# Performance work log

Hardware: AMD Instinct MI355X
Metric: run time of the kernel (lower is better)

The kernel has to match this reference:

```python
import jax, jax.numpy as jnp
import numpy as np
import math

N_MENTIONS = 8192
EMB = 1024


def setup_inputs() -> dict:
    key = jax.random.key(0)
    k0, k1, k2 = jax.random.split(key, 3)
    scale = 1.0 / math.sqrt(EMB)
    return {
        "all_mentions": jax.random.normal(k0, (N_MENTIONS, EMB), dtype=jnp.float32),
        "Wq": jax.random.normal(k1, (EMB, EMB), dtype=jnp.float32) * scale,
        "bq": jnp.zeros((EMB,), dtype=jnp.float32),
        "Wk": jax.random.normal(k2, (EMB, EMB), dtype=jnp.float32) * scale,
        "bk": jnp.zeros((EMB,), dtype=jnp.float32),
    }


def reference(all_mentions, Wq, bq, Wk, bk):
    # torch.nn.Linear: y = x @ W.T + b
    E = all_mentions.shape[-1]
    q = (all_mentions @ Wq.T + bq) / jnp.sqrt(jnp.asarray(E, all_mentions.dtype))
    k = all_mentions @ Wk.T + bk
    # [N, N] raw attention logits
    attn = q @ k.T
    # causal mask: -inf strictly above the diagonal (triu, diagonal=1)
    n = all_mentions.shape[0]
    mask = jnp.where(jnp.triu(jnp.ones((n, n), dtype=bool), k=1),
                     jnp.asarray(-jnp.inf, attn.dtype),
                     jnp.asarray(0.0, attn.dtype))
    # Module returns attn_weights = masked pre-softmax logits (single layer,
    # single head, bsz=1); the softmax@v branch is discarded by the caller.
    return attn + mask
```

## Files before the change

kernel.cpp:

```cpp
#include <hip/hip_runtime.h>
#include <math.h>

#define NM 8192
#define KDIM 1024

#define NEG_BIG (-3.0e38f)

typedef __attribute__((ext_vector_type(4))) float floatx4;
typedef __attribute__((ext_vector_type(8))) _Float16 halfx8;
typedef __attribute__((ext_vector_type(4))) _Float16 halfx4;

#define SMEM_BYTES (3 * (256 * 64 + 128 * 64) * 2)

__device__ __forceinline__ void gload_lds16(const void* g, void* l) {
    __builtin_amdgcn_global_load_lds(
        (const __attribute__((address_space(1))) void*)g,
        (__attribute__((address_space(3))) void*)l,
        16, 0, 0);
}

__global__ __launch_bounds__(256)
void convert_kernel(const float* __restrict__ X,
                    const float* __restrict__ Wq,
                    const float* __restrict__ Wk,
                    _Float16* __restrict__ Xf,
                    _Float16* __restrict__ Wqf,
                    _Float16* __restrict__ Wkf) {
    const int XB = (NM * KDIM) / 4 / 256;
    const int WB = (KDIM * KDIM) / 4 / 256;
    int b = blockIdx.x;
    const float* src;
    _Float16* dst;
    if (b < XB)            { src = X;  dst = Xf; }
    else if (b < XB + WB)  { b -= XB;       src = Wq; dst = Wqf; }
    else                   { b -= XB + WB;  src = Wk; dst = Wkf; }
    const int i = b * 256 + threadIdx.x;
    floatx4 v = ((const floatx4*)src)[i];
    halfx4 h;
    h.x = (_Float16)v.x;
    h.y = (_Float16)v.y;
    h.z = (_Float16)v.z;
    h.w = (_Float16)v.w;
    *(halfx4*)&dst[(size_t)i * 4] = h;
}


#define GEMM_PIPE_BODY(APTR, BPTR)                                            \
    extern __shared__ _Float16 smem[];                                        \
    _Float16* const sAl = smem;                           \
    _Float16* const sBl = smem + 3 * 16384;               \
    const int t = threadIdx.x;                                                \
    const int lane = t & 63;                                                  \
    const int quad = lane >> 4;                                               \
    const int l15 = lane & 15;                                                \
    const int wv = t >> 6;                                                    \
    const int wr = (wv >> 1) * 64;                \
    const int wc = (wv & 1) * 64;                 \
    const int srow = t >> 3;             \
    const int skoff = ((t & 7) ^ ((t >> 3) & 7)) * 8;     \
    auto stA = [&](int kt, int pb, int c) {                                   \
        gload_lds16(APTR + (size_t)(row0 + c * 64 + srow) * KDIM              \
                         + kt * 64 + skoff,                                   \
                    sAl + pb * 16384 + (c * 512 + t) * 8);                    \
    };                                                                        \
    auto stB = [&](int kt, int pb, int c) {                                   \
        gload_lds16(BPTR + (size_t)(col0 + c * 64 + srow) * KDIM              \
                         + kt * 64 + skoff,                                   \
                    sBl + pb * 8192 + (c * 512 + t) * 8);                     \
    };                                                                        \
    floatx4 acc[4][4];                                                        \
    _Pragma("unroll")                                                         \
    for (int i = 0; i < 4; i++)                                               \
        _Pragma("unroll")                                                     \
        for (int j = 0; j < 4; j++) acc[i][j] = (floatx4){0.f, 0.f, 0.f, 0.f}; \
    stA(0, 0, 0); stA(0, 0, 1); stA(0, 0, 2); stA(0, 0, 3);                   \
    stB(0, 0, 0); stB(0, 0, 1);                                               \
    stA(1, 1, 0); stA(1, 1, 1); stA(1, 1, 2); stA(1, 1, 3);                   \
    stB(1, 1, 0); stB(1, 1, 1);                                               \
    asm volatile("s_waitcnt vmcnt(6)" ::: "memory");       \
    __builtin_amdgcn_s_barrier();                                             \
    _Pragma("unroll")                                                         \
    for (int kt = 0; kt < 16; ++kt) {                                         \
        const int pb = kt % 3;                                                \
        const int pq = (kt + 2) % 3;                                          \
        halfx8 a[4], b[4];                                                    \
                                              \
        if (kt < 14) { stA(kt + 2, pq, 0); stA(kt + 2, pq, 1);                \
                       stB(kt + 2, pq, 0); }                                  \
        _Pragma("unroll")                                                     \
        for (int i = 0; i < 4; i++) {                                         \
            const int r = wr + i * 16 + l15;                                  \
            a[i] = *(const halfx8*)&sAl[pb * 16384 + r * 64 +                 \
                                        ((quad ^ (r & 7)) * 8)];              \
        }                                                                     \
        _Pragma("unroll")                                                     \
        for (int j = 0; j < 4; j++) {                                         \
            const int r = wc + j * 16 + l15;                                  \
            b[j] = *(const halfx8*)&sBl[pb * 8192 + r * 64 +                  \
                                        ((quad ^ (r & 7)) * 8)];              \
        }                                                                     \
        __builtin_amdgcn_s_barrier();                                         \
        asm volatile("s_waitcnt lgkmcnt(0)" ::: "memory");                    \
        __builtin_amdgcn_sched_barrier(0);                                    \
        __builtin_amdgcn_s_setprio(1);                                        \
        _Pragma("unroll")                                                     \
        for (int j = 0; j < 4; j++)                                           \
            _Pragma("unroll")                                                 \
            for (int i = 0; i < 4; i++)                                       \
                acc[i][j] = __builtin_amdgcn_mfma_f32_16x16x32_f16(           \
                    a[i], b[j], acc[i][j], 0, 0, 0);                          \
        __builtin_amdgcn_s_setprio(0);                                        \
        __builtin_amdgcn_s_barrier();                                         \
                                              \
        if (kt < 14) { stA(kt + 2, pq, 2); stA(kt + 2, pq, 3);                \
                       stB(kt + 2, pq, 1); }                                  \
        _Pragma("unroll")                                                     \
        for (int i = 0; i < 4; i++) {                                         \
            const int r = wr + i * 16 + l15;                                  \
            a[i] = *(const halfx8*)&sAl[pb * 16384 + r * 64 +                 \
                                        (((4 + quad) ^ (r & 7)) * 8)];        \
        }                                                                     \
        _Pragma("unroll")                                                     \
        for (int j = 0; j < 4; j++) {                                         \
            const int r = wc + j * 16 + l15;                                  \
            b[j] = *(const halfx8*)&sBl[pb * 8192 + r * 64 +                  \
                                        (((4 + quad) ^ (r & 7)) * 8)];        \
        }                                                                     \
        __builtin_amdgcn_s_barrier();                                         \
        asm volatile("s_waitcnt lgkmcnt(0)" ::: "memory");                    \
        __builtin_amdgcn_sched_barrier(0);                                    \
        __builtin_amdgcn_s_setprio(1);                                        \
        _Pragma("unroll")                                                     \
        for (int j = 0; j < 4; j++)                                           \
            _Pragma("unroll")                                                 \
            for (int i = 0; i < 4; i++)                                       \
                acc[i][j] = __builtin_amdgcn_mfma_f32_16x16x32_f16(           \
                    a[i], b[j], acc[i][j], 0, 0, 0);                          \
        __builtin_amdgcn_s_setprio(0);                                        \
        if (kt < 14)       asm volatile("s_waitcnt vmcnt(6)" ::: "memory");   \
        else if (kt == 14) asm volatile("s_waitcnt vmcnt(0)" ::: "memory");   \
        if (kt < 15) __builtin_amdgcn_s_barrier();                            \
    }

__global__ __launch_bounds__(512, 2)
void proj_kernel(const _Float16* __restrict__ Xf,
                 const _Float16* __restrict__ Wqf, const float* __restrict__ bq,
                 _Float16* __restrict__ Qf,
                 const _Float16* __restrict__ Wkf, const float* __restrict__ bk,
                 _Float16* __restrict__ Kf) {
    const bool isK = (blockIdx.z == 1);
    const _Float16* W    = isK ? Wkf : Wqf;
    const float*    bias = isK ? bk : bq;
    _Float16*       O    = isK ? Kf : Qf;
    const float scale = isK ? 1.0f : 0.03125f;

    const int row0 = blockIdx.y * 256;
    const int col0 = blockIdx.x * 128;

    GEMM_PIPE_BODY(Xf, W)

#pragma unroll
    for (int i = 0; i < 4; i++)
#pragma unroll
        for (int j = 0; j < 4; j++)
#pragma unroll
            for (int r = 0; r < 4; r++) {
                const int grow = row0 + wr + i * 16 + quad * 4 + r;
                const int gcol = col0 + wc + j * 16 + l15;
                const float v = (acc[i][j][r] + bias[gcol]) * scale;
                O[(size_t)grow * KDIM + gcol] = (_Float16)v;
            }
}

__global__ __launch_bounds__(512, 2)
void attn_kernel(const _Float16* __restrict__ Qf,
                 const _Float16* __restrict__ Kf,
                 float* __restrict__ out) {
    const int lid = blockIdx.x;
    const int x = lid & 7;
    const int s = lid >> 3;
    const int bi = s & 31;
    const int bj = ((s >> 5) << 3) + x;

    if (bj * 128 > bi * 256 + 255) {
        const int tid = threadIdx.x;
        const floatx4 v = {NEG_BIG, NEG_BIG, NEG_BIG, NEG_BIG};
        floatx4* o4 = (floatx4*)(out + (size_t)bi * 256 * NM + (size_t)bj * 128);
#pragma unroll
        for (int it = 0; it < 16; ++it) {
            const int idx = it * 512 + tid;
            const int r = idx >> 5;
            const int c = idx & 31;
            __builtin_nontemporal_store(v, &o4[(size_t)r * (NM / 4) + c]);
        }
        return;
    }

    const int row0 = bi * 256;
    const int col0 = bj * 128;

    GEMM_PIPE_BODY(Qf, Kf)

#pragma unroll
    for (int i = 0; i < 4; i++)
#pragma unroll
        for (int j = 0; j < 4; j++)
#pragma unroll
            for (int r = 0; r < 4; r++) {
                const int grow = row0 + wr + i * 16 + quad * 4 + r;
                const int gcol = col0 + wc + j * 16 + l15;
                const float v = (gcol <= grow) ? acc[i][j][r] : NEG_BIG;
                __builtin_nontemporal_store(v, &out[(size_t)grow * NM + gcol]);
            }
}

extern "C" void kernel_launch(void* const* d_in, const int* in_sizes, int n_in,
                              void* d_out, int out_size, void* d_ws, size_t ws_size,
                              hipStream_t stream) {
    const float* X  = (const float*)d_in[0];
    const float* Wq = (const float*)d_in[1];
    const float* bq = (const float*)d_in[2];
    const float* Wk = (const float*)d_in[3];
    const float* bk = (const float*)d_in[4];
    float* out = (float*)d_out;

    _Float16* p = (_Float16*)d_ws;
    const size_t XN = (size_t)NM * KDIM;
    const size_t WN = (size_t)KDIM * KDIM;
    _Float16* Xf  = p;  p += XN;
    _Float16* Wqf = p;  p += WN;
    _Float16* Wkf = p;  p += WN;
    _Float16* Qf  = p;  p += XN;
    _Float16* Kf  = p;  p += XN;

    static bool attr_done = false;
    if (!attr_done) {
        hipFuncSetAttribute((const void*)proj_kernel,
                            hipFuncAttributeMaxDynamicSharedMemorySize, SMEM_BYTES);
        hipFuncSetAttribute((const void*)attn_kernel,
                            hipFuncAttributeMaxDynamicSharedMemorySize, SMEM_BYTES);
        attr_done = true;
    }

    const int nconv = (int)((XN + 2 * WN) / 4 / 256);
    convert_kernel<<<nconv, 256, 0, stream>>>(X, Wq, Wk, Xf, Wqf, Wkf);

    dim3 pgrid(KDIM / 128, NM / 256, 2);
    proj_kernel<<<pgrid, 512, SMEM_BYTES, stream>>>(Xf, Wqf, bq, Qf, Wkf, bk, Kf);

    attn_kernel<<<(NM / 256) * (NM / 128), 512, SMEM_BYTES, stream>>>(Qf, Kf, out);
}
```

Baseline: 434.4 us.

## Switch GEMMs to 256x256 tiles with 8-phase double-buffered pipeline

Both the projection and attention GEMMs move from 256x128 block tiles with a 3-stage LDS ring to 256x256 tiles with a 2-stage double buffer. Each K-tile is split into four phases that interleave LDS reads, async global-to-LDS staging and MFMA bursts. This raises arithmetic intensity per block and halves the number of blocks. The causal skip test becomes a block-level bj > bi check, and masking is applied only on diagonal tiles. In exchange it uses more accumulator registers, does coarser diagonal work, and the pipeline timing is tighter with only two buffers.

```diff
diff --git a/kernel.cpp b/kernel.cpp
--- a/kernel.cpp
+++ b/kernel.cpp
@@ -10,7 +10,7 @@
 typedef __attribute__((ext_vector_type(8))) _Float16 halfx8;
 typedef __attribute__((ext_vector_type(4))) _Float16 halfx4;
 
-#define SMEM_BYTES (3 * (256 * 64 + 128 * 64) * 2)
+#define SMEM_BYTES (2 * 2 * 256 * 64 * 2)
 
 __device__ __forceinline__ void gload_lds16(const void* g, void* l) {
     __builtin_amdgcn_global_load_lds(
@@ -45,101 +45,138 @@
 }
 
 
-#define GEMM_PIPE_BODY(APTR, BPTR)                                            \
+#define RD_A(d, i, kk)                                                        \
+    (*(const halfx8*)&smem[(d) * 32768 + ((i) >> 2) * 8192 +                  \
+                           (((i) & 3) * 32 + wm * 16 + l15) * 64 +            \
+                           ((((kk) * 4 + quad) ^ (l15 & 7)) * 8)])
+#define RD_B(d, j, kk)                                                        \
+    (*(const halfx8*)&smem[(d) * 32768 + 16384 + ((j) >> 1) * 8192 +          \
+                           (((j) & 1) * 64 + wn * 16 + l15) * 64 +            \
+                           ((((kk) * 4 + quad) ^ (l15 & 7)) * 8)])
+
+#define MFMA16(JLO, JHI, IOFF)                                                \
+    _Pragma("unroll")                                                         \
+    for (int jj = (JLO); jj < (JHI); ++jj)                                    \
+        _Pragma("unroll")                                                     \
+        for (int ii = 0; ii < 4; ++ii) {                                      \
+            acc[(IOFF) + ii][jj] = __builtin_amdgcn_mfma_f32_16x16x32_f16(    \
+                aR[ii][0], bR[jj][0], acc[(IOFF) + ii][jj], 0, 0, 0);         \
+            acc[(IOFF) + ii][jj] = __builtin_amdgcn_mfma_f32_16x16x32_f16(    \
+                aR[ii][1], bR[jj][1], acc[(IOFF) + ii][jj], 0, 0, 0);         \
+        }
+
+#define KTILE(d, STG1, STG2, STG3, STG4, VMTAIL)                              \
+    {                                                                         \
+                                                       \
+        _Pragma("unroll")                                                     \
+        for (int ii = 0; ii < 4; ++ii) {                                      \
+            aR[ii][0] = RD_A(d, ii, 0);                                       \
+            aR[ii][1] = RD_A(d, ii, 1);                                       \
+        }                                                                     \
+        _Pragma("unroll")                                                     \
+        for (int jj = 0; jj < 2; ++jj) {                                      \
+            bR[jj][0] = RD_B(d, jj, 0);                                       \
+            bR[jj][1] = RD_B(d, jj, 1);                                       \
+        }                                                                     \
+        STG1;                                                                 \
+        asm volatile("s_waitcnt lgkmcnt(8)" ::: "memory");                    \
+        __builtin_amdgcn_s_barrier();                                         \
+        asm volatile("s_waitcnt lgkmcnt(0)" ::: "memory");                    \
+        __builtin_amdgcn_sched_barrier(0);                                    \
+        __builtin_amdgcn_s_setprio(1);                                        \
+        MFMA16(0, 2, 0)                                                       \
+        __builtin_amdgcn_s_setprio(0);                                        \
+        __builtin_amdgcn_s_barrier();                                         \
+                                                       \
+        _Pragma("unroll")                                                     \
+        for (int jj = 2; jj < 4; ++jj) {                                      \
+            bR[jj][0] = RD_B(d, jj, 0);                                       \
+            bR[jj][1] = RD_B(d, jj, 1);                                       \
+        }                                                                     \
+        STG2;                                                                 \
+        __builtin_amdgcn_s_barrier();                                         \
+        asm volatile("s_waitcnt lgkmcnt(0)" ::: "memory");                    \
+        __builtin_amdgcn_sched_barrier(0);                                    \
+        __builtin_amdgcn_s_setprio(1);                                        \
+        MFMA16(2, 4, 0)                                                       \
+        __builtin_amdgcn_s_setprio(0);                                        \
+        __builtin_amdgcn_s_barrier();                                         \
+                                                       \
+        _Pragma("unroll")                                                     \
+        for (int ii = 0; ii < 4; ++ii) {                                      \
+            aR[ii][0] = RD_A(d, 4 + ii, 0);                                   \
+            aR[ii][1] = RD_A(d, 4 + ii, 1);                                   \
+        }                                                                     \
+        STG3;                                                                 \
+        __builtin_amdgcn_s_barrier();                                         \
+        asm volatile("s_waitcnt lgkmcnt(0)" ::: "memory");                    \
+        __builtin_amdgcn_sched_barrier(0);                                    \
+        __builtin_amdgcn_s_setprio(1);                                        \
+        MFMA16(0, 2, 4)                                                       \
+        __builtin_amdgcn_s_setprio(0);                                        \
+        __builtin_amdgcn_s_barrier();                                         \
+                                \
+        STG4;                                                                 \
+        __builtin_amdgcn_s_barrier();                                         \
+        __builtin_amdgcn_s_setprio(1);                                        \
+        MFMA16(2, 4, 4)                                                       \
+        __builtin_amdgcn_s_setprio(0);                                        \
+        VMTAIL;                                                               \
+        __builtin_amdgcn_s_barrier();                                         \
+    }
+
+#define GEMM_CORE_8PHASE(APTR, BPTR)                                          \
     extern __shared__ _Float16 smem[];                                        \
-    _Float16* const sAl = smem;                           \
-    _Float16* const sBl = smem + 3 * 16384;               \
     const int t = threadIdx.x;                                                \
     const int lane = t & 63;                                                  \
     const int quad = lane >> 4;                                               \
     const int l15 = lane & 15;                                                \
-    const int wv = t >> 6;                                                    \
-    const int wr = (wv >> 1) * 64;                \
-    const int wc = (wv & 1) * 64;                 \
-    const int srow = t >> 3;             \
-    const int skoff = ((t & 7) ^ ((t >> 3) & 7)) * 8;     \
-    auto stA = [&](int kt, int pb, int c) {                                   \
-        gload_lds16(APTR + (size_t)(row0 + c * 64 + srow) * KDIM              \
-                         + kt * 64 + skoff,                                   \
-                    sAl + pb * 16384 + (c * 512 + t) * 8);                    \
+    const int wm = (t >> 6) >> 2;                                             \
+    const int wn = (t >> 6) & 3;                                              \
+    const int srow8 = t >> 3;                                                 \
+    const int schunk = ((t & 7) ^ (srow8 & 7)) * 8;                           \
+    const _Float16* const aSrc = (APTR) + (size_t)(row0 + srow8) * KDIM + schunk; \
+    const _Float16* const bSrc = (BPTR) + (size_t)(col0 + srow8) * KDIM + schunk; \
+    auto STG_A = [&](int kt, int d, int h) {                                  \
+        _Pragma("unroll")                                                     \
+        for (int c = 0; c < 2; ++c)                                           \
+            gload_lds16(aSrc + (size_t)(h * 128 + c * 64) * KDIM + kt * 64,   \
+                        smem + d * 32768 + h * 8192 + (c * 512 + t) * 8);     \
     };                                                                        \
-    auto stB = [&](int kt, int pb, int c) {                                   \
-        gload_lds16(BPTR + (size_t)(col0 + c * 64 + srow) * KDIM              \
-                         + kt * 64 + skoff,                                   \
-                    sBl + pb * 8192 + (c * 512 + t) * 8);                     \
+    auto STG_B = [&](int kt, int d, int h) {                                  \
+        _Pragma("unroll")                                                     \
+        for (int c = 0; c < 2; ++c)                                           \
+            gload_lds16(bSrc + (size_t)(h * 128 + c * 64) * KDIM + kt * 64,   \
+                        smem + d * 32768 + 16384 + h * 8192 + (c * 512 + t) * 8); \
     };                                                                        \
-    floatx4 acc[4][4];                                                        \
+    floatx4 acc[8][4];                                                        \
     _Pragma("unroll")                                                         \
-    for (int i = 0; i < 4; i++)                                               \
+    for (int i = 0; i < 8; i++)                                               \
         _Pragma("unroll")                                                     \
         for (int j = 0; j < 4; j++) acc[i][j] = (floatx4){0.f, 0.f, 0.f, 0.f}; \
-    stA(0, 0, 0); stA(0, 0, 1); stA(0, 0, 2); stA(0, 0, 3);                   \
-    stB(0, 0, 0); stB(0, 0, 1);                                               \
-    stA(1, 1, 0); stA(1, 1, 1); stA(1, 1, 2); stA(1, 1, 3);                   \
-    stB(1, 1, 0); stB(1, 1, 1);                                               \
-    asm volatile("s_waitcnt vmcnt(6)" ::: "memory");       \
+    halfx8 aR[4][2], bR[4][2];                                                \
+          \
+    STG_A(0, 0, 0); STG_B(0, 0, 0); STG_B(0, 0, 1); STG_A(0, 0, 1);           \
+    STG_A(1, 1, 0); STG_B(1, 1, 0); STG_B(1, 1, 1);                           \
+    asm volatile("s_waitcnt vmcnt(6)" ::: "memory");          \
     __builtin_amdgcn_s_barrier();                                             \
-    _Pragma("unroll")                                                         \
-    for (int kt = 0; kt < 16; ++kt) {                                         \
-        const int pb = kt % 3;                                                \
-        const int pq = (kt + 2) % 3;                                          \
-        halfx8 a[4], b[4];                                                    \
-                                              \
-        if (kt < 14) { stA(kt + 2, pq, 0); stA(kt + 2, pq, 1);                \
-                       stB(kt + 2, pq, 0); }                                  \
-        _Pragma("unroll")                                                     \
-        for (int i = 0; i < 4; i++) {                                         \
-            const int r = wr + i * 16 + l15;                                  \
-            a[i] = *(const halfx8*)&sAl[pb * 16384 + r * 64 +                 \
-                                        ((quad ^ (r & 7)) * 8)];              \
-        }                                                                     \
-        _Pragma("unroll")                                                     \
-        for (int j = 0; j < 4; j++) {                                         \
-            const int r = wc + j * 16 + l15;                                  \
-            b[j] = *(const halfx8*)&sBl[pb * 8192 + r * 64 +                  \
-                                        ((quad ^ (r & 7)) * 8)];              \
-        }                                                                     \
-        __builtin_amdgcn_s_barrier();                                         \
-        asm volatile("s_waitcnt lgkmcnt(0)" ::: "memory");                    \
-        __builtin_amdgcn_sched_barrier(0);                                    \
-        __builtin_amdgcn_s_setprio(1);                                        \
-        _Pragma("unroll")                                                     \
-        for (int j = 0; j < 4; j++)                                           \
-            _Pragma("unroll")                                                 \
-            for (int i = 0; i < 4; i++)                                       \
-                acc[i][j] = __builtin_amdgcn_mfma_f32_16x16x32_f16(           \
-                    a[i], b[j], acc[i][j], 0, 0, 0);                          \
-        __builtin_amdgcn_s_setprio(0);                                        \
-        __builtin_amdgcn_s_barrier();                                         \
-                                              \
-        if (kt < 14) { stA(kt + 2, pq, 2); stA(kt + 2, pq, 3);                \
-                       stB(kt + 2, pq, 1); }                                  \
-        _Pragma("unroll")                                                     \
-        for (int i = 0; i < 4; i++) {                                         \
-            const int r = wr + i * 16 + l15;                                  \
-            a[i] = *(const halfx8*)&sAl[pb * 16384 + r * 64 +                 \
-                                        (((4 + quad) ^ (r & 7)) * 8)];        \
-        }                                                                     \
-        _Pragma("unroll")                                                     \
-        for (int j = 0; j < 4; j++) {                                         \
-            const int r = wc + j * 16 + l15;                                  \
-            b[j] = *(const halfx8*)&sBl[pb * 8192 + r * 64 +                  \
-                                        (((4 + quad) ^ (r & 7)) * 8)];        \
-        }                                                                     \
-        __builtin_amdgcn_s_barrier();                                         \
-        asm volatile("s_waitcnt lgkmcnt(0)" ::: "memory");                    \
-        __builtin_amdgcn_sched_barrier(0);                                    \
-        __builtin_amdgcn_s_setprio(1);                                        \
-        _Pragma("unroll")                                                     \
-        for (int j = 0; j < 4; j++)                                           \
-            _Pragma("unroll")                                                 \
-            for (int i = 0; i < 4; i++)                                       \
-                acc[i][j] = __builtin_amdgcn_mfma_f32_16x16x32_f16(           \
-                    a[i], b[j], acc[i][j], 0, 0, 0);                          \
-        __builtin_amdgcn_s_setprio(0);                                        \
-        if (kt < 14)       asm volatile("s_waitcnt vmcnt(6)" ::: "memory");   \
-        else if (kt == 14) asm volatile("s_waitcnt vmcnt(0)" ::: "memory");   \
-        if (kt < 15) __builtin_amdgcn_s_barrier();                            \
+    _Pragma("unroll 1")                                                       \
+    for (int it = 0; it < 8; ++it) {                                          \
+        const int kt1 = 2 * it + 1, kt2 = 2 * it + 2, kt3 = 2 * it + 3;       \
+        const bool stg = (it < 7);                                            \
+        KTILE(0,                                                              \
+              STG_A(kt1, 1, 1),                                               \
+              if (stg) STG_A(kt2, 0, 0),                                      \
+              if (stg) STG_B(kt2, 0, 0),                                      \
+              if (stg) STG_B(kt2, 0, 1),                                      \
+              if (stg) { asm volatile("s_waitcnt vmcnt(6)" ::: "memory"); }   \
+              else { asm volatile("s_waitcnt vmcnt(0)" ::: "memory"); })      \
+        KTILE(1,                                                              \
+              if (stg) STG_A(kt2, 0, 1),                                      \
+              if (stg) STG_A(kt3, 1, 0),                                      \
+              if (stg) STG_B(kt3, 1, 0),                                      \
+              if (stg) STG_B(kt3, 1, 1),                                      \
+              if (stg) { asm volatile("s_waitcnt vmcnt(6)" ::: "memory"); })  \
     }
 
 __global__ __launch_bounds__(512, 2)
@@ -155,19 +192,19 @@
     const float scale = isK ? 1.0f : 0.03125f;
 
     const int row0 = blockIdx.y * 256;
-    const int col0 = blockIdx.x * 128;
-
-    GEMM_PIPE_BODY(Xf, W)
-
-#pragma unroll
-    for (int i = 0; i < 4; i++)
+    const int col0 = blockIdx.x * 256;
+
+    GEMM_CORE_8PHASE(Xf, W)
+
+#pragma unroll
+    for (int i = 0; i < 8; i++)
 #pragma unroll
         for (int j = 0; j < 4; j++)
 #pragma unroll
-            for (int r = 0; r < 4; r++) {
-                const int grow = row0 + wr + i * 16 + quad * 4 + r;
-                const int gcol = col0 + wc + j * 16 + l15;
-                const float v = (acc[i][j][r] + bias[gcol]) * scale;
+            for (int rr = 0; rr < 4; rr++) {
+                const int grow = row0 + i * 32 + wm * 16 + quad * 4 + rr;
+                const int gcol = col0 + j * 64 + wn * 16 + l15;
+                const float v = (acc[i][j][rr] + bias[gcol]) * scale;
                 O[(size_t)grow * KDIM + gcol] = (_Float16)v;
             }
 }
@@ -182,34 +219,35 @@
     const int bi = s & 31;
     const int bj = ((s >> 5) << 3) + x;
 
-    if (bj * 128 > bi * 256 + 255) {
+    if (bj > bi) {
         const int tid = threadIdx.x;
         const floatx4 v = {NEG_BIG, NEG_BIG, NEG_BIG, NEG_BIG};
-        floatx4* o4 = (floatx4*)(out + (size_t)bi * 256 * NM + (size_t)bj * 128);
-#pragma unroll
-        for (int it = 0; it < 16; ++it) {
-            const int idx = it * 512 + tid;
-            const int r = idx >> 5;
-            const int c = idx & 31;
+        floatx4* o4 = (floatx4*)(out + (size_t)bi * 256 * NM + (size_t)bj * 256);
+#pragma unroll
+        for (int itf = 0; itf < 32; ++itf) {
+            const int idx = itf * 512 + tid;
+            const int r = idx >> 6;
+            const int c = idx & 63;
             __builtin_nontemporal_store(v, &o4[(size_t)r * (NM / 4) + c]);
         }
         return;
     }
 
     const int row0 = bi * 256;
-    const int col0 = bj * 128;
-
-    GEMM_PIPE_BODY(Qf, Kf)
-
-#pragma unroll
-    for (int i = 0; i < 4; i++)
+    const int col0 = bj * 256;
+    const bool diag = (bi == bj);
+
+    GEMM_CORE_8PHASE(Qf, Kf)
+
+#pragma unroll
+    for (int i = 0; i < 8; i++)
 #pragma unroll
         for (int j = 0; j < 4; j++)
 #pragma unroll
-            for (int r = 0; r < 4; r++) {
-                const int grow = row0 + wr + i * 16 + quad * 4 + r;
-                const int gcol = col0 + wc + j * 16 + l15;
-                const float v = (gcol <= grow) ? acc[i][j][r] : NEG_BIG;
+            for (int rr = 0; rr < 4; rr++) {
+                const int grow = row0 + i * 32 + wm * 16 + quad * 4 + rr;
+                const int gcol = col0 + j * 64 + wn * 16 + l15;
+                const float v = (!diag || gcol <= grow) ? acc[i][j][rr] : NEG_BIG;
                 __builtin_nontemporal_store(v, &out[(size_t)grow * NM + gcol]);
             }
 }
@@ -245,8 +283,8 @@
     const int nconv = (int)((XN + 2 * WN) / 4 / 256);
     convert_kernel<<<nconv, 256, 0, stream>>>(X, Wq, Wk, Xf, Wqf, Wkf);
 
-    dim3 pgrid(KDIM / 128, NM / 256, 2);
+    dim3 pgrid(KDIM / 256, NM / 256, 2);
     proj_kernel<<<pgrid, 512, SMEM_BYTES, stream>>>(Xf, Wqf, bq, Qf, Wkf, bk, Kf);
 
-    attn_kernel<<<(NM / 256) * (NM / 128), 512, SMEM_BYTES, stream>>>(Qf, Kf, out);
-}
+    attn_kernel<<<(NM / 256) * (NM / 256), 512, SMEM_BYTES, stream>>>(Qf, Kf, out);
+}
```

New measurement: 424.2 us. 1.02x faster.
